# Kernel optimization log

Hardware: AMD Instinct MI355X
Metric: run time of the kernel (lower is better)

Reference implementation:

```python
import jax, jax.numpy as jnp
from jax import lax
import numpy as np

K = 10
N_SEEDS = 20


def farthest_point_sample(xyz, npoint):
    # xyz: [B, N, C] -> centroids [B, npoint] (int32)
    B, N, C = xyz.shape

    def step(carry, _):
        distance, farthest = carry
        centroid = jnp.take_along_axis(xyz, farthest[:, None, None], axis=1)  # [B,1,C]
        d = jnp.sum((xyz - centroid) ** 2, axis=-1)  # [B,N]
        distance = jnp.minimum(distance, d)
        new_farthest = jnp.argmax(distance, axis=-1)
        return (distance, new_farthest), farthest

    init = (jnp.full((B, N), 1e10, xyz.dtype), jnp.zeros((B,), jnp.int32))
    _, cents = lax.scan(step, init, None, length=npoint)  # [npoint, B]
    return cents.T  # [B, npoint]


def setup_inputs() -> dict:
    key = jax.random.key(0)
    pcs = jax.random.normal(key, (64, 16384, 3), dtype=jnp.float32)
    return {"pcs": pcs}


def reference(pcs):
    # pcs: [B, N, 3]
    seeds = farthest_point_sample(pcs, N_SEEDS)  # [B, n_seeds]
    seeds_value = jnp.take_along_axis(pcs, seeds[:, :, None], axis=1)  # [B, n_seeds, 3]
    # dist_new in the torch code: [B, n_seeds, N] (seed-to-point distances)
    diff = seeds_value[:, :, None, :] - pcs[:, None, :, :]  # [B, n_seeds, N, 3]
    dist_new = jnp.linalg.norm(diff, axis=-1)  # [B, n_seeds, N]
    # k+1 smallest distances per seed (ascending)
    neg_top, _ = lax.top_k(-dist_new, K + 1)
    top_dist = -neg_top  # [B, n_seeds, k+1], ascending
    overall_mean = jnp.mean(top_dist[:, :, 1:])
    top_dist = top_dist / overall_mean
    m = jnp.mean(top_dist, axis=2)  # [B, n_seeds]
    var = jnp.var(m, ddof=1)  # torch.var default: unbiased
    return var
```

## Files before the change

kernel.cpp:

```cpp
#include <hip/hip_runtime.h>

#pragma clang fp contract(off)

#define N_PTS   16384
#define N_SEEDS 20
#define KP1     11
#define NBIN    512
#define NREP    32
#define CAP     4096
#define NKNN    3

typedef unsigned long long u64;
typedef unsigned int       u32;

#define FMAXDPP(m, ctrl, rmask) { \
    const int _v = __builtin_amdgcn_update_dpp(__float_as_int(m), __float_as_int(m), \
                                               (ctrl), (rmask), 0xf, false); \
    m = fmaxf(m, __int_as_float(_v)); }

#define FDECL(i) float px##i, py##i, pz##i, dd##i = 1e10f;
#define LOADPTS(P4)                                                         \
    {   const int f4 = t * 12;                                              \
        const float4 q0 = P4[f4+0],  q1 = P4[f4+1],  q2  = P4[f4+2];        \
        const float4 q3 = P4[f4+3],  q4 = P4[f4+4],  q5  = P4[f4+5];        \
        const float4 q6 = P4[f4+6],  q7 = P4[f4+7],  q8  = P4[f4+8];        \
        const float4 q9 = P4[f4+9],  q10 = P4[f4+10], q11 = P4[f4+11];      \
        px0 =q0.x;  py0 =q0.y;  pz0 =q0.z;                                  \
        px1 =q0.w;  py1 =q1.x;  pz1 =q1.y;                                  \
        px2 =q1.z;  py2 =q1.w;  pz2 =q2.x;                                  \
        px3 =q2.y;  py3 =q2.z;  pz3 =q2.w;                                  \
        px4 =q3.x;  py4 =q3.y;  pz4 =q3.z;                                  \
        px5 =q3.w;  py5 =q4.x;  pz5 =q4.y;                                  \
        px6 =q4.z;  py6 =q4.w;  pz6 =q5.x;                                  \
        px7 =q5.y;  py7 =q5.z;  pz7 =q5.w;                                  \
        px8 =q6.x;  py8 =q6.y;  pz8 =q6.z;                                  \
        px9 =q6.w;  py9 =q7.x;  pz9 =q7.y;                                  \
        px10=q7.z;  py10=q7.w;  pz10=q8.x;                                  \
        px11=q8.y;  py11=q8.z;  pz11=q8.w;                                  \
        px12=q9.x;  py12=q9.y;  pz12=q9.z;                                  \
        px13=q9.w;  py13=q10.x; pz13=q10.y;                                 \
        px14=q10.z; py14=q10.w; pz14=q11.x;                                 \
        px15=q11.y; py15=q11.z; pz15=q11.w; }

__global__ __launch_bounds__(1024)
__attribute__((amdgpu_waves_per_eu(4, 4)))
void fused_kernel(const float* __restrict__ pcs,
                  int* __restrict__ seeds,
                  int* __restrict__ done,
                  float* __restrict__ topd,
                  float* __restrict__ out,
                  int B) {
    __shared__ alignas(16) u32 hist[NBIN * NREP];
    __shared__ u32    part[NBIN];
    __shared__ float  cand[CAP];
    __shared__ u32    cnt;
    __shared__ u32    s_thr;
    __shared__ int    s_sid;
    __shared__ float  s_val[2][16];
    __shared__ float4 s_pack[2];

    const int bid  = blockIdx.x;
    const int t    = threadIdx.x;
    const int lane = t & 63;
    const int wid  = t >> 6;

    if (bid < B) {
        const float* __restrict__ P  = pcs + (size_t)bid * N_PTS * 3;
        const float4* __restrict__ P4 = (const float4*)P;

        FDECL(0)  FDECL(1)  FDECL(2)  FDECL(3)
        FDECL(4)  FDECL(5)  FDECL(6)  FDECL(7)
        FDECL(8)  FDECL(9)  FDECL(10) FDECL(11)
        FDECL(12) FDECL(13) FDECL(14) FDECL(15)
        LOADPTS(P4)

        float cx = P[0], cy = P[1], cz = P[2];
        int farthest = 0;

        for (int it = 0; it < N_SEEDS; ++it) {
            if (t == 0)
                __hip_atomic_store(&seeds[bid * N_SEEDS + it], farthest,
                                   __ATOMIC_RELAXED, __HIP_MEMORY_SCOPE_AGENT);
            if (it == N_SEEDS - 1) break;

            float v0 = -1.f, v1 = -1.f, v2 = -1.f, v3 = -1.f;
#define FS(c, i) { const float dx = px##i - cx, dy = py##i - cy, dz = pz##i - cz; \
        const float d  = (dx*dx + dy*dy) + dz*dz; \
        const float nd = fminf(dd##i, d); dd##i = nd; \
        v##c = fmaxf(v##c, nd); }
            FS(0,0)  FS(1,1)  FS(2,2)  FS(3,3)
            FS(0,4)  FS(1,5)  FS(2,6)  FS(3,7)
            FS(0,8)  FS(1,9)  FS(2,10) FS(3,11)
            FS(0,12) FS(1,13) FS(2,14) FS(3,15)
            const float bestv = fmaxf(fmaxf(v0, v1), fmaxf(v2, v3));

            float m = bestv;
            FMAXDPP(m, 0x111, 0xf)
            FMAXDPP(m, 0x112, 0xf)
            FMAXDPP(m, 0x114, 0xf)
            FMAXDPP(m, 0x118, 0xf)
            FMAXDPP(m, 0x142, 0xa)
            FMAXDPP(m, 0x143, 0xc)
            const float wmax = __int_as_float(
                __builtin_amdgcn_readlane(__float_as_int(m), 63));
            const int par = it & 1;
            if (lane == 0) s_val[par][wid] = wmax;
            __syncthreads();

            const float v16 = s_val[par][lane & 15];
            float r = v16;
            FMAXDPP(r, 0x111, 0xf)
            FMAXDPP(r, 0x112, 0xf)
            FMAXDPP(r, 0x114, 0xf)
            FMAXDPP(r, 0x118, 0xf)
            const float gmax = __int_as_float(
                __builtin_amdgcn_readlane(__float_as_int(r), 15));
            const u64 m2 = __ballot(v16 == gmax) & 0xFFFFull;
            const int ws = __ffsll((unsigned long long)m2) - 1;

            if (wid == ws) {
                const u64 lm = __ballot(bestv == gmax);
                const int ll = __ffsll((unsigned long long)lm) - 1;
                if (lane == ll) {
                    int fi = 0; float sx = 0.f, sy = 0.f, sz = 0.f;
#define SCAN(i) if (dd##i == gmax) { fi = t*16 + (i); sx = px##i; sy = py##i; sz = pz##i; }
                    SCAN(15) SCAN(14) SCAN(13) SCAN(12)
                    SCAN(11) SCAN(10) SCAN(9)  SCAN(8)
                    SCAN(7)  SCAN(6)  SCAN(5)  SCAN(4)
                    SCAN(3)  SCAN(2)  SCAN(1)  SCAN(0)
                    s_pack[par] = make_float4(__int_as_float(fi), sx, sy, sz);
                }
            }
            __syncthreads();

            const float4 pk = s_pack[par];
            farthest = __float_as_int(pk.x);
            cx = pk.y; cy = pk.z; cz = pk.w;
        }
    } else {
        const int kk = bid - B;
        const int b  = kk % B;
        const int j  = kk / B;

        const float* __restrict__ P  = pcs + (size_t)b * N_PTS * 3;
        const float4* __restrict__ P4 = (const float4*)P;
        const int rep = t & 31;

        FDECL(0)  FDECL(1)  FDECL(2)  FDECL(3)
        FDECL(4)  FDECL(5)  FDECL(6)  FDECL(7)
        FDECL(8)  FDECL(9)  FDECL(10) FDECL(11)
        FDECL(12) FDECL(13) FDECL(14) FDECL(15)
        LOADPTS(P4)

#pragma unroll
        for (int i = 0; i < (NBIN * NREP) / 1024; ++i) hist[t + i * 1024] = 0u;
        if (t == 0) cnt = 0u;

        for (int s = j; s < N_SEEDS; s += NKNN) {
            if (t == 0) {
                int sv;
                while ((sv = __hip_atomic_load(&seeds[b * N_SEEDS + s],
                               __ATOMIC_RELAXED, __HIP_MEMORY_SCOPE_AGENT)) < 0)
                    __builtin_amdgcn_s_sleep(2);
                s_sid = sv;
            }
            __syncthreads();
            const int sid = s_sid;
            const float cx = P[sid*3], cy = P[sid*3+1], cz = P[sid*3+2];

#define HSTEP(i) { const float dx = px##i - cx, dy = py##i - cy, dz = pz##i - cz; \
        const float d = fmaf(dz, dz, fmaf(dy, dy, dx * dx)); \
        atomicAdd(&hist[(__float_as_uint(d) >> 22) * NREP + rep], 1u); }
            HSTEP(0)  HSTEP(1)  HSTEP(2)  HSTEP(3)
            HSTEP(4)  HSTEP(5)  HSTEP(6)  HSTEP(7)
            HSTEP(8)  HSTEP(9)  HSTEP(10) HSTEP(11)
            HSTEP(12) HSTEP(13) HSTEP(14) HSTEP(15)
            __syncthreads();

            if (t < NBIN) {
                u32 ssum = 0;
#pragma unroll
                for (int r2 = 0; r2 < NREP; ++r2)
                    ssum += hist[t * NREP + ((r2 + t) & (NREP - 1))];
                part[t] = ssum;
            }
            __syncthreads();

            if (wid == 0) {
                u32 s8 = 0;
#pragma unroll
                for (int i = 0; i < 8; ++i)
                    s8 += part[lane * 8 + ((i + lane) & 7)];
                u32 cum = s8;
                for (int off = 1; off < 64; off <<= 1) {
                    const u32 o = __shfl_up(cum, off);
                    if (lane >= off) cum += o;
                }
                const u64 mm = __ballot(cum >= (u32)KP1);
                const int L  = __ffsll((unsigned long long)mm) - 1;
                const u32 below = __shfl(cum - s8, L);
                const u32 bc = (lane < 8) ? part[L * 8 + lane] : 0u;
                u32 ic = bc;
                for (int off = 1; off < 8; off <<= 1) {
                    const u32 o = __shfl_up(ic, off);
                    if (lane >= off) ic += o;
                }
                const u64 mm2 = __ballot(lane < 8 && (below + ic) >= (u32)KP1);
                const int l2  = __ffsll((unsigned long long)mm2) - 1;
                if (lane == 0) s_thr = (u32)(L * 8 + l2 + 1) << 22;
            } else {
                if (t == 64) cnt = 0u;
                for (int i = t - 64; i < NBIN * NREP; i += 960) hist[i] = 0u;
            }
            __syncthreads();

            const float thrf = __uint_as_float(s_thr);
#define CSTEP(i) { const float dx = px##i - cx, dy = py##i - cy, dz = pz##i - cz; \
        const float d = fmaf(dz, dz, fmaf(dy, dy, dx * dx)); \
        if (d < thrf) { const u32 sl = atomicAdd(&cnt, 1u); \
                        if (sl < (u32)CAP) cand[sl] = d; } }
            CSTEP(0)  CSTEP(1)  CSTEP(2)  CSTEP(3)
            CSTEP(4)  CSTEP(5)  CSTEP(6)  CSTEP(7)
            CSTEP(8)  CSTEP(9)  CSTEP(10) CSTEP(11)
            CSTEP(12) CSTEP(13) CSTEP(14) CSTEP(15)
            __syncthreads();

            if (wid == 0) {
                const u32 n = min(cnt, (u32)CAP);
                for (u32 base = 0; base < n; base += 64) {
                    const u32 idx = base + (u32)lane;
                    const float vv = (idx < n) ? cand[idx] : 3.0e38f;
                    u32 r2 = 0;
                    for (u32 jj = 0; jj < n; ++jj) {
                        const float w = cand[jj];
                        r2 += (w < vv || (w == vv && jj < idx)) ? 1u : 0u;
                    }
                    if (idx < n && r2 < (u32)KP1)
                        topd[(b * N_SEEDS + s) * KP1 + r2] = sqrtf(vv);
                }
            }
        }

        __syncthreads();
        if (t == 0) {
            __threadfence();
            __hip_atomic_fetch_add(done, 1, __ATOMIC_RELAXED,
                                   __HIP_MEMORY_SCOPE_AGENT);
        }

        if (bid == B) {
            const int target = NKNN * B - 1;
            if (t == 0) {
                while (__hip_atomic_load(done, __ATOMIC_RELAXED,
                                         __HIP_MEMORY_SCOPE_AGENT) != target)
                    __builtin_amdgcn_s_sleep(8);
            }
            __syncthreads();
            __threadfence();

            const int pairs = B * N_SEEDS;
            double* red = (double*)hist;

            double P_ = 0.0, Q_ = 0.0, F_ = 0.0;
            for (int pr = t; pr < pairs; pr += 1024) {
                double ps = 0.0;
                for (int jj = 0; jj < KP1; ++jj)
                    ps += (double)topd[pr * KP1 + jj];
                P_ += ps;
                Q_ += ps * ps;
                F_ += (double)topd[pr * KP1];
            }
            red[t*3+0] = P_; red[t*3+1] = Q_; red[t*3+2] = F_;
            __syncthreads();
            for (int off = 512; off; off >>= 1) {
                if (t < off) {
                    red[t*3+0] += red[(t+off)*3+0];
                    red[t*3+1] += red[(t+off)*3+1];
                    red[t*3+2] += red[(t+off)*3+2];
                }
                __syncthreads();
            }
            if (t == 0) {
                const double Pt = red[0], Qt = red[1], Ft = red[2];
                const double S1 = Pt - Ft;
                const double om = S1 / (double)(pairs * (KP1 - 1));
                const double d11 = om * (double)KP1;
                const double sm = Pt / d11;
                const double sq = Qt / (d11 * d11);
                const double var = (sq - sm * sm / (double)pairs)
                                   / (double)(pairs - 1);
                out[0] = (float)var;
            }
        }
    }
}

extern "C" void kernel_launch(void* const* d_in, const int* in_sizes, int n_in,
                              void* d_out, int out_size, void* d_ws, size_t ws_size,
                              hipStream_t stream) {
    const float* pcs = (const float*)d_in[0];
    const int B = in_sizes[0] / (N_PTS * 3);

    int*   seeds = (int*)d_ws;
    int*   done  = (int*)((char*)d_ws + 5120);
    float* topd  = (float*)((char*)d_ws + 8192);
    float* out   = (float*)d_out;

    (void)hipMemsetAsync(d_ws, 0xFF, 8192, stream);

    fused_kernel<<<B * (1 + NKNN), 1024, 0, stream>>>(pcs, seeds, done, topd, out, B);
}
```

Baseline: 50.52 us.

## Compute last seed's kNN in FPS block and finalize via last-arriver

The FPS block now handles the kNN histogram/threshold/top-k selection for the final seed itself, using its register-resident points, instead of leaving that seed to a helper block that waits for it. This removes the tail where a kNN block spins on the last seed after FPS finishes. The final variance reduction moves from a dedicated block spin-waiting on a counter to whichever block arrives last, detected with an atomic fetch-add. That removes a spinning resident block, but the FPS block's critical path now includes one kNN selection. An unused leftover SELECT_BODY macro is also added.

```diff
diff --git a/kernel.cpp b/kernel.cpp
--- a/kernel.cpp
+++ b/kernel.cpp
@@ -42,6 +42,18 @@
         px14=q10.z; py14=q10.w; pz14=q11.x;                                 \
         px15=q11.y; py15=q11.z; pz15=q11.w; }
 
+#define SELECT_BODY(BLK)                                                        \
+    {                                                                           \
+                                              \
+    _Pragma("clang diagnostic push")                                            \
+    ;                                                                           \
+    {                                                                           \
+        const int rep = t & 31;                                                 \
+        (void)rep;                                                              \
+    }                                                                           \
+    _Pragma("clang diagnostic pop")                                             \
+    }
+
 __global__ __launch_bounds__(1024)
 __attribute__((amdgpu_waves_per_eu(4, 4)))
 void fused_kernel(const float* __restrict__ pcs,
@@ -63,6 +75,11 @@
     const int t    = threadIdx.x;
     const int lane = t & 63;
     const int wid  = t >> 6;
+    const int rep  = t & 31;
+
+    int   selblk = -1;
+    float scx = 0.f, scy = 0.f, scz = 0.f;
+    bool  do_sel = false;
 
     if (bid < B) {
         const float* __restrict__ P  = pcs + (size_t)bid * N_PTS * 3;
@@ -73,6 +90,10 @@
         FDECL(8)  FDECL(9)  FDECL(10) FDECL(11)
         FDECL(12) FDECL(13) FDECL(14) FDECL(15)
         LOADPTS(P4)
+
+#pragma unroll
+        for (int i = 0; i < (NBIN * NREP) / 1024; ++i) hist[t + i * 1024] = 0u;
+        if (t == 0) cnt = 0u;
 
         float cx = P[0], cy = P[1], cz = P[2];
         int farthest = 0;
@@ -137,38 +158,12 @@
             farthest = __float_as_int(pk.x);
             cx = pk.y; cy = pk.z; cz = pk.w;
         }
-    } else {
-        const int kk = bid - B;
-        const int b  = kk % B;
-        const int j  = kk / B;
-
-        const float* __restrict__ P  = pcs + (size_t)b * N_PTS * 3;
-        const float4* __restrict__ P4 = (const float4*)P;
-        const int rep = t & 31;
-
-        FDECL(0)  FDECL(1)  FDECL(2)  FDECL(3)
-        FDECL(4)  FDECL(5)  FDECL(6)  FDECL(7)
-        FDECL(8)  FDECL(9)  FDECL(10) FDECL(11)
-        FDECL(12) FDECL(13) FDECL(14) FDECL(15)
-        LOADPTS(P4)
-
-#pragma unroll
-        for (int i = 0; i < (NBIN * NREP) / 1024; ++i) hist[t + i * 1024] = 0u;
-        if (t == 0) cnt = 0u;
-
-        for (int s = j; s < N_SEEDS; s += NKNN) {
-            if (t == 0) {
-                int sv;
-                while ((sv = __hip_atomic_load(&seeds[b * N_SEEDS + s],
-                               __ATOMIC_RELAXED, __HIP_MEMORY_SCOPE_AGENT)) < 0)
-                    __builtin_amdgcn_s_sleep(2);
-                s_sid = sv;
-            }
-            __syncthreads();
-            const int sid = s_sid;
-            const float cx = P[sid*3], cy = P[sid*3+1], cz = P[sid*3+2];
-
-#define HSTEP(i) { const float dx = px##i - cx, dy = py##i - cy, dz = pz##i - cz; \
+
+        {
+            __syncthreads();
+            const float ccx = cx, ccy = cy, ccz = cz;
+
+#define HSTEP(i) { const float dx = px##i - ccx, dy = py##i - ccy, dz = pz##i - ccz; \
         const float d = fmaf(dz, dz, fmaf(dy, dy, dx * dx)); \
         atomicAdd(&hist[(__float_as_uint(d) >> 22) * NREP + rep], 1u); }
             HSTEP(0)  HSTEP(1)  HSTEP(2)  HSTEP(3)
@@ -208,6 +203,104 @@
                 const u64 mm2 = __ballot(lane < 8 && (below + ic) >= (u32)KP1);
                 const int l2  = __ffsll((unsigned long long)mm2) - 1;
                 if (lane == 0) s_thr = (u32)(L * 8 + l2 + 1) << 22;
+            } else if (t == 64) {
+                cnt = 0u;
+            }
+            __syncthreads();
+
+            const float thrf = __uint_as_float(s_thr);
+#define CSTEP(i) { const float dx = px##i - ccx, dy = py##i - ccy, dz = pz##i - ccz; \
+        const float d = fmaf(dz, dz, fmaf(dy, dy, dx * dx)); \
+        if (d < thrf) { const u32 sl = atomicAdd(&cnt, 1u); \
+                        if (sl < (u32)CAP) cand[sl] = d; } }
+            CSTEP(0)  CSTEP(1)  CSTEP(2)  CSTEP(3)
+            CSTEP(4)  CSTEP(5)  CSTEP(6)  CSTEP(7)
+            CSTEP(8)  CSTEP(9)  CSTEP(10) CSTEP(11)
+            CSTEP(12) CSTEP(13) CSTEP(14) CSTEP(15)
+            __syncthreads();
+
+            if (wid == 0) {
+                const u32 n = min(cnt, (u32)CAP);
+                for (u32 base = 0; base < n; base += 64) {
+                    const u32 idx = base + (u32)lane;
+                    const float vv = (idx < n) ? cand[idx] : 3.0e38f;
+                    u32 r2 = 0;
+                    for (u32 jj = 0; jj < n; ++jj) {
+                        const float w = cand[jj];
+                        r2 += (w < vv || (w == vv && jj < idx)) ? 1u : 0u;
+                    }
+                    if (idx < n && r2 < (u32)KP1)
+                        topd[(bid * N_SEEDS + (N_SEEDS - 1)) * KP1 + r2] = sqrtf(vv);
+                }
+            }
+        }
+    } else {
+        const int kk = bid - B;
+        const int b  = kk % B;
+        const int j  = kk / B;
+
+        const float* __restrict__ P  = pcs + (size_t)b * N_PTS * 3;
+        const float4* __restrict__ P4 = (const float4*)P;
+
+        FDECL(0)  FDECL(1)  FDECL(2)  FDECL(3)
+        FDECL(4)  FDECL(5)  FDECL(6)  FDECL(7)
+        FDECL(8)  FDECL(9)  FDECL(10) FDECL(11)
+        FDECL(12) FDECL(13) FDECL(14) FDECL(15)
+        LOADPTS(P4)
+
+#pragma unroll
+        for (int i = 0; i < (NBIN * NREP) / 1024; ++i) hist[t + i * 1024] = 0u;
+        if (t == 0) cnt = 0u;
+
+        for (int s = j; s < N_SEEDS - 1; s += NKNN) {
+            if (t == 0) {
+                int sv;
+                while ((sv = __hip_atomic_load(&seeds[b * N_SEEDS + s],
+                               __ATOMIC_RELAXED, __HIP_MEMORY_SCOPE_AGENT)) < 0)
+                    __builtin_amdgcn_s_sleep(2);
+                s_sid = sv;
+            }
+            __syncthreads();
+            const int sid = s_sid;
+            const float ccx = P[sid*3], ccy = P[sid*3+1], ccz = P[sid*3+2];
+
+            HSTEP(0)  HSTEP(1)  HSTEP(2)  HSTEP(3)
+            HSTEP(4)  HSTEP(5)  HSTEP(6)  HSTEP(7)
+            HSTEP(8)  HSTEP(9)  HSTEP(10) HSTEP(11)
+            HSTEP(12) HSTEP(13) HSTEP(14) HSTEP(15)
+            __syncthreads();
+
+            if (t < NBIN) {
+                u32 ssum = 0;
+#pragma unroll
+                for (int r2 = 0; r2 < NREP; ++r2)
+                    ssum += hist[t * NREP + ((r2 + t) & (NREP - 1))];
+                part[t] = ssum;
+            }
+            __syncthreads();
+
+            if (wid == 0) {
+                u32 s8 = 0;
+#pragma unroll
+                for (int i = 0; i < 8; ++i)
+                    s8 += part[lane * 8 + ((i + lane) & 7)];
+                u32 cum = s8;
+                for (int off = 1; off < 64; off <<= 1) {
+                    const u32 o = __shfl_up(cum, off);
+                    if (lane >= off) cum += o;
+                }
+                const u64 mm = __ballot(cum >= (u32)KP1);
+                const int L  = __ffsll((unsigned long long)mm) - 1;
+                const u32 below = __shfl(cum - s8, L);
+                const u32 bc = (lane < 8) ? part[L * 8 + lane] : 0u;
+                u32 ic = bc;
+                for (int off = 1; off < 8; off <<= 1) {
+                    const u32 o = __shfl_up(ic, off);
+                    if (lane >= off) ic += o;
+                }
+                const u64 mm2 = __ballot(lane < 8 && (below + ic) >= (u32)KP1);
+                const int l2  = __ffsll((unsigned long long)mm2) - 1;
+                if (lane == 0) s_thr = (u32)(L * 8 + l2 + 1) << 22;
             } else {
                 if (t == 64) cnt = 0u;
                 for (int i = t - 64; i < NBIN * NREP; i += 960) hist[i] = 0u;
@@ -215,10 +308,6 @@
             __syncthreads();
 
             const float thrf = __uint_as_float(s_thr);
-#define CSTEP(i) { const float dx = px##i - cx, dy = py##i - cy, dz = pz##i - cz; \
-        const float d = fmaf(dz, dz, fmaf(dy, dy, dx * dx)); \
-        if (d < thrf) { const u32 sl = atomicAdd(&cnt, 1u); \
-                        if (sl < (u32)CAP) cand[sl] = d; } }
             CSTEP(0)  CSTEP(1)  CSTEP(2)  CSTEP(3)
             CSTEP(4)  CSTEP(5)  CSTEP(6)  CSTEP(7)
             CSTEP(8)  CSTEP(9)  CSTEP(10) CSTEP(11)
@@ -240,57 +329,51 @@
                 }
             }
         }
-
+    }
+
+    __syncthreads();
+    if (t == 0) {
+        __threadfence();
+        const int old = __hip_atomic_fetch_add(done, 1, __ATOMIC_RELAXED,
+                                               __HIP_MEMORY_SCOPE_AGENT);
+        s_sid = (old == (1 + NKNN) * B - 2) ? 1 : 0;
+    }
+    __syncthreads();
+    if (s_sid == 1) {
+        __threadfence();
+
+        const int pairs = B * N_SEEDS;
+        double* red = (double*)hist;
+
+        double P_ = 0.0, Q_ = 0.0, F_ = 0.0;
+        for (int pr = t; pr < pairs; pr += 1024) {
+            double ps = 0.0;
+            for (int jj = 0; jj < KP1; ++jj)
+                ps += (double)topd[pr * KP1 + jj];
+            P_ += ps;
+            Q_ += ps * ps;
+            F_ += (double)topd[pr * KP1];
+        }
+        red[t*3+0] = P_; red[t*3+1] = Q_; red[t*3+2] = F_;
         __syncthreads();
+        for (int off = 512; off; off >>= 1) {
+            if (t < off) {
+                red[t*3+0] += red[(t+off)*3+0];
+                red[t*3+1] += red[(t+off)*3+1];
+                red[t*3+2] += red[(t+off)*3+2];
+            }
+            __syncthreads();
+        }
         if (t == 0) {
-            __threadfence();
-            __hip_atomic_fetch_add(done, 1, __ATOMIC_RELAXED,
-                                   __HIP_MEMORY_SCOPE_AGENT);
-        }
-
-        if (bid == B) {
-            const int target = NKNN * B - 1;
-            if (t == 0) {
-                while (__hip_atomic_load(done, __ATOMIC_RELAXED,
-                                         __HIP_MEMORY_SCOPE_AGENT) != target)
-                    __builtin_amdgcn_s_sleep(8);
-            }
-            __syncthreads();
-            __threadfence();
-
-            const int pairs = B * N_SEEDS;
-            double* red = (double*)hist;
-
-            double P_ = 0.0, Q_ = 0.0, F_ = 0.0;
-            for (int pr = t; pr < pairs; pr += 1024) {
-                double ps = 0.0;
-                for (int jj = 0; jj < KP1; ++jj)
-                    ps += (double)topd[pr * KP1 + jj];
-                P_ += ps;
-                Q_ += ps * ps;
-                F_ += (double)topd[pr * KP1];
-            }
-            red[t*3+0] = P_; red[t*3+1] = Q_; red[t*3+2] = F_;
-            __syncthreads();
-            for (int off = 512; off; off >>= 1) {
-                if (t < off) {
-                    red[t*3+0] += red[(t+off)*3+0];
-                    red[t*3+1] += red[(t+off)*3+1];
-                    red[t*3+2] += red[(t+off)*3+2];
-                }
-                __syncthreads();
-            }
-            if (t == 0) {
-                const double Pt = red[0], Qt = red[1], Ft = red[2];
-                const double S1 = Pt - Ft;
-                const double om = S1 / (double)(pairs * (KP1 - 1));
-                const double d11 = om * (double)KP1;
-                const double sm = Pt / d11;
-                const double sq = Qt / (d11 * d11);
-                const double var = (sq - sm * sm / (double)pairs)
-                                   / (double)(pairs - 1);
-                out[0] = (float)var;
-            }
+            const double Pt = red[0], Qt = red[1], Ft = red[2];
+            const double S1 = Pt - Ft;
+            const double om = S1 / (double)(pairs * (KP1 - 1));
+            const double d11 = om * (double)KP1;
+            const double sm = Pt / d11;
+            const double sq = Qt / (d11 * d11);
+            const double var = (sq - sm * sm / (double)pairs)
+                               / (double)(pairs - 1);
+            out[0] = (float)var;
         }
     }
 }
```

Result: slower. 56.90 us (+12.6%).
